# Kernel tuning notes

Hardware: AMD Instinct MI355X
Metric: run time of the kernel (lower is better)

Reference implementation:

```python
import jax, jax.numpy as jnp
import numpy as np
from jax import lax

# ---- module config (init_kwargs) ----
B, CIN, COUT, H, W, K = 16, 32, 32, 256, 256, 3
FEATURE_BITS = 8
INPUT_ZP = 3
OUTPUT_ZP = -5
INPUT_SCALE = 0.02
OUTPUT_SCALE = 0.05
STRIDE = (1, 1)
PAD_H, PAD_W = 1, 1
DILATION = (1, 1)
GROUPS = 1
QMIN, QMAX = -(2 ** (FEATURE_BITS - 1)), 2 ** (FEATURE_BITS - 1) - 1  # -128, 127


def float_to_fixed_point(scale, bitwidth):
    # Represent scale (in (0,1)) as int_scale * 2^-frac_bits with int_scale <= 2^(b-1)-1.
    # Pick the largest frac_bits s.t. round(scale * 2^frac_bits) fits -> max precision.
    qmax = jnp.float32(2 ** (bitwidth - 1) - 1)
    frac_bits = jnp.floor(jnp.log2(qmax / scale)).astype(jnp.int32)
    int_scale = jnp.round(scale * jnp.exp2(frac_bits.astype(jnp.float32))).astype(jnp.int32)
    return int_scale, frac_bits


def setup_inputs() -> dict:
    key = jax.random.key(0)
    k0, k1, k2, k3 = jax.random.split(key, 4)
    x = jax.random.randint(k0, (B, CIN, H, W), -128, 128, dtype=jnp.int32).astype(jnp.int8)
    qweight = jax.random.randint(k1, (COUT, CIN, K, K), -128, 128, dtype=jnp.int32).astype(jnp.int8)
    qbias = jax.random.randint(k2, (COUT,), -1000, 1000, dtype=jnp.int32)
    weight_scale = jax.random.uniform(k3, (COUT,), jnp.float32, 1e-3, 1e-2)
    return {"x": x, "qweight": qweight, "qbias": qbias, "weight_scale": weight_scale}


def reference(x, qweight, qbias, weight_scale):
    # F.pad(qinput, (pw,pw,ph,ph), 'constant', input_zero_point) -> pad W and H dims
    xp = jnp.pad(x, ((0, 0), (0, 0), (PAD_H, PAD_H), (PAD_W, PAD_W)),
                 mode="constant", constant_values=INPUT_ZP)
    # int32 conv (no bias), VALID since input was pre-padded
    out = lax.conv_general_dilated(
        xp.astype(jnp.int32), qweight.astype(jnp.int32),
        window_strides=STRIDE, padding="VALID", rhs_dilation=DILATION,
        dimension_numbers=("NCHW", "OIHW", "NCHW"), feature_group_count=GROUPS)
    # shifted bias: qbias - sum(qweight) * input_zero_point  (per out channel)
    shifted_qbias = qbias - qweight.astype(jnp.int32).sum((1, 2, 3)) * INPUT_ZP
    out = out + shifted_qbias[None, :, None, None]
    # fixed-point requant: (out * int_scale) >> frac_bits, per channel
    folded_scale = (INPUT_SCALE * weight_scale / OUTPUT_SCALE).astype(jnp.float32)
    int_scale, frac_bits = float_to_fixed_point(folded_scale, FEATURE_BITS)
    out = jnp.right_shift(out * int_scale[None, :, None, None],
                          frac_bits[None, :, None, None])  # arithmetic shift on int32
    out = out + OUTPUT_ZP
    out = jnp.clip(out, QMIN, QMAX).astype(jnp.int8)
    return out
```

## Files before the change

kernel.cpp:

```cpp
#include <hip/hip_runtime.h>

#define B_   16
#define CIN  32
#define COUT 32
#define H_   256
#define W_   256
#define IN_ZP  3
#define OUT_ZP (-5)
#define HW (H_ * W_)
#define TH 8
#define TW 64
#define SW 72
#define SH 10

#define XPH 258
#define XPW 264
#define XPQ 66
#define PLANE_W (XPH * XPW)
#define XP_WORDS (B_ * 8 * PLANE_W)
#define WS_TAB 2400
#define WS_NEED ((size_t)(WS_TAB + XP_WORDS) * 4)
#define NQ (B_ * 8 * XPH * XPQ)
#define PACK_BLOCKS 2176


using i32x4  = __attribute__((ext_vector_type(4))) int;
using i32x16 = __attribute__((ext_vector_type(16))) int;


__global__ __launch_bounds__(256) void qconv_pack(const int* __restrict__ x,
                                                  const int* __restrict__ qw,
                                                  const int* __restrict__ qb,
                                                  const float* __restrict__ wscale,
                                                  int* __restrict__ ws) {
    const int bid = blockIdx.x;
    const int tid = threadIdx.x;
    if (bid < 32) {
        __shared__ int red[4];
        const int co = bid;
        const int* wco = qw + co * (CIN * 9);
        int s = 0;
        for (int i = tid; i < CIN * 9; i += 256) s += wco[i];
        for (int off = 32; off; off >>= 1) s += __shfl_down(s, off, 64);
        if ((tid & 63) == 0) red[tid >> 6] = s;

        if (tid < 72) {
            int gidx = co * 72 + tid;
            int g    = gidx & 3;
            int lane = (gidx >> 2) & 63;
            int t    = gidx >> 8;
            int wco2 = lane & 31;
            int ci0  = 16 * (lane >> 5) + 4 * g;
            const int* base = qw + wco2 * (CIN * 9);
            int b0 = base[(ci0 + 0) * 9 + t] & 0xff;
            int b1 = base[(ci0 + 1) * 9 + t] & 0xff;
            int b2 = base[(ci0 + 2) * 9 + t] & 0xff;
            int b3 = base[(ci0 + 3) * 9 + t] & 0xff;
            ws[gidx] = b0 | (b1 << 8) | (b2 << 16) | (b3 << 24);
        }
        __syncthreads();
        if (tid == 0) {
            int wsum = red[0] + red[1] + red[2] + red[3];
            int sb   = qb[co] - wsum * IN_ZP;
            float fs = (0.02f * wscale[co]) / 0.05f;
            float fb = floorf(log2f(127.0f / fs));
            int isc  = (int)rintf(fs * exp2f(fb));
            int ifb  = (int)fb;
            ws[2304 + co] = sb * isc + OUT_ZP * (1 << ifb);
            ws[2336 + co] = isc;
            ws[2368 + co] = ifb;
        }
        return;
    }
    int* __restrict__ xp = ws + WS_TAB;
    const int T = (PACK_BLOCKS) * 256;
    for (int q = (bid - 32) * 256 + tid; q < NQ; q += T) {
        int b   = q / (8 * XPH * XPQ);
        int r1  = q - b * (8 * XPH * XPQ);
        int cig = r1 / (XPH * XPQ);
        int r2  = r1 - cig * (XPH * XPQ);
        int ph  = r2 / XPQ;
        int cq  = r2 - ph * XPQ;
        int gh  = ph - 1;
        int gw0 = cq * 4 - 4;
        int ghc = min(H_ - 1, max(0, gh));
        int gwc = min(W_ - 4, max(0, gw0));
        const int* p = x + (b * CIN + cig * 4) * HW + ghc * W_ + gwc;
        i32x4 v0 = *(const i32x4*)(p);
        i32x4 v1 = *(const i32x4*)(p + HW);
        i32x4 v2 = *(const i32x4*)(p + 2 * HW);
        i32x4 v3 = *(const i32x4*)(p + 3 * HW);
        bool vh = (unsigned)gh < (unsigned)H_;
        i32x4 pk;
#pragma unroll
        for (int j = 0; j < 4; ++j) {
            int t = (v0[j] & 0xff) | ((v1[j] & 0xff) << 8) |
                    ((v2[j] & 0xff) << 16) | (v3[j] << 24);
            bool ok = vh && ((unsigned)(gw0 + j) < (unsigned)W_);
            pk[j] = ok ? t : 0x03030303;
        }
        *(i32x4*)(xp + 4 * q) = pk;
    }
}

__global__ __launch_bounds__(256) void qconv_fused(const int* __restrict__ ws,
                                                   int* __restrict__ out) {
    __shared__ __align__(16) int cons[96];

    const int d  = blockIdx.x + 4 * blockIdx.y + 128 * blockIdx.z;
    const int w  = ((d & 7) << 8) | (d >> 3);
    const int tx = w & 3;
    const int ty = (w >> 2) & 31;
    const int tb = w >> 7;

    const int wt = tx * TW;
    const int ht = ty * TH;
    const int tid = threadIdx.x;
    const int lane = tid & 63, wv = tid >> 6;
    const int hh  = lane >> 5;
    const int pix = lane & 31;
    const int* __restrict__ xp = ws + WS_TAB;

    if (tid < 96) cons[tid] = ws[2304 + tid];

    i32x4 wfrag[9];
    const i32x4* wsv = (const i32x4*)ws;
#pragma unroll
    for (int t = 0; t < 9; ++t) wfrag[t] = wsv[t * 64 + lane];

    __syncthreads();

    const int rowbase = (tb * 8) * XPH + ht;
    const int* xbase = xp + rowbase * XPW + wt + pix + 3;

#pragma unroll 1
    for (int i = 0; i < 4; ++i) {
        const int mt = wv * 4 + i;
        const int r0 = mt >> 1, chunk = mt & 1;
        const int* xt = xbase + (hh * 4) * PLANE_W + r0 * XPW + chunk * 32;
        i32x16 acc;
#pragma unroll
        for (int r = 0; r < 16; ++r) acc[r] = 0;
#pragma unroll
        for (int dh = 0; dh < 3; ++dh) {
#pragma unroll
            for (int dw = 0; dw < 3; ++dw) {
                i32x4 a;
#pragma unroll
                for (int g = 0; g < 4; ++g)
                    a[g] = xt[g * PLANE_W + dh * XPW + dw];
                acc = __builtin_amdgcn_mfma_i32_32x32x32_i8(
                          wfrag[dh * 3 + dw], a, acc, 0, 0, 0);
            }
        }
        int* op = out + (tb * COUT) * HW + (ht + r0) * W_ + wt + chunk * 32 + pix;
#pragma unroll
        for (int rg = 0; rg < 4; ++rg) {
            const int cb = 4 * hh + 8 * rg;
            i32x4 sbi4 = *(const i32x4*)&cons[cb];
            i32x4 isc4 = *(const i32x4*)&cons[32 + cb];
            i32x4 fb4  = *(const i32x4*)&cons[64 + cb];
#pragma unroll
            for (int j = 0; j < 4; ++j) {
                int v = (__mul24(acc[rg * 4 + j], isc4[j]) + sbi4[j]) >> fb4[j];
                v = min(127, max(-128, v));
                __builtin_nontemporal_store(v, op + (cb + j) * HW);
            }
        }
    }
}

__global__ void qconv_prep_fb(const int* __restrict__ qw, const int* __restrict__ qb,
                              const float* __restrict__ wscale, int* __restrict__ ws) {
    const int co  = blockIdx.x;
    const int tid = threadIdx.x;
    __shared__ int red[4];
    const int* wco = qw + co * (CIN * 9);
    int s = 0;
    for (int i = tid; i < CIN * 9; i += 256) s += wco[i];
    for (int off = 32; off; off >>= 1) s += __shfl_down(s, off, 64);
    if ((tid & 63) == 0) red[tid >> 6] = s;
    if (tid < 72) {
        int gidx = blockIdx.x * 72 + tid;
        int g    = gidx & 3;
        int lane = (gidx >> 2) & 63;
        int t    = gidx >> 8;
        int wco2 = lane & 31;
        int ci0  = 16 * (lane >> 5) + 4 * g;
        const int* base = qw + wco2 * (CIN * 9);
        int b0 = base[(ci0 + 0) * 9 + t] & 0xff;
        int b1 = base[(ci0 + 1) * 9 + t] & 0xff;
        int b2 = base[(ci0 + 2) * 9 + t] & 0xff;
        int b3 = base[(ci0 + 3) * 9 + t] & 0xff;
        ws[gidx] = b0 | (b1 << 8) | (b2 << 16) | (b3 << 24);
    }
    __syncthreads();
    if (tid == 0) {
        int wsum = red[0] + red[1] + red[2] + red[3];
        ws[2304 + co] = qb[co] - wsum * IN_ZP;
        float fs = (0.02f * wscale[co]) / 0.05f;
        float fb = floorf(log2f(127.0f / fs));
        int isc = (int)rintf(fs * exp2f(fb));
        ws[2336 + co] = isc | (((int)fb) << 16);
    }
}

__device__ __forceinline__ void stage_item(int idx, int ht, int wt,
                                           const int* __restrict__ xb,
                                           int (*smem)[SH][SW]) {
    int cig = idx / 180;
    int rem = idx - cig * 180;
    int r   = rem / 18;
    int c4  = rem - r * 18;
    int gh  = ht - 1 + r;
    int gw0 = wt - 4 + c4 * 4;
    int ghc = min(H_ - 1, max(0, gh));
    int gwc = min(W_ - 4, max(0, gw0));
    const int* p = xb + (cig * 4) * HW + ghc * W_ + gwc;
    i32x4 v0 = *(const i32x4*)(p);
    i32x4 v1 = *(const i32x4*)(p + HW);
    i32x4 v2 = *(const i32x4*)(p + 2 * HW);
    i32x4 v3 = *(const i32x4*)(p + 3 * HW);
    bool vh = (unsigned)gh < (unsigned)H_;
    i32x4 pk;
#pragma unroll
    for (int j = 0; j < 4; ++j) {
        int t = (v0[j] & 0xff) | ((v1[j] & 0xff) << 8) |
                ((v2[j] & 0xff) << 16) | (v3[j] << 24);
        bool ok = vh && ((unsigned)(gw0 + j) < (unsigned)W_);
        pk[j] = ok ? t : 0x03030303;
    }
    *(i32x4*)&smem[cig][r][c4 * 4] = pk;
}

__global__ __launch_bounds__(256) void qconv_fused_fb(const int* __restrict__ x,
                                                      const int* __restrict__ ws,
                                                      int* __restrict__ out) {
    __shared__ int smem[8][SH][SW];
    __shared__ __align__(16) int cons[64];
    const int d  = blockIdx.x + 4 * blockIdx.y + 128 * blockIdx.z;
    const int w  = ((d & 7) << 8) | (d >> 3);
    const int tx = w & 3;
    const int ty = (w >> 2) & 31;
    const int tb = w >> 7;
    const int wt = tx * TW;
    const int ht = ty * TH;
    const int tid = threadIdx.x;
    const int* xb = x + tb * (CIN * HW);
    if (tid < 64) cons[tid] = ws[2304 + tid];
    stage_item(tid,        ht, wt, xb, smem);
    stage_item(tid + 256,  ht, wt, xb, smem);
    stage_item(tid + 512,  ht, wt, xb, smem);
    stage_item(tid + 768,  ht, wt, xb, smem);
    stage_item(tid + 1024, ht, wt, xb, smem);
    if (tid < 160) stage_item(tid + 1280, ht, wt, xb, smem);
    __syncthreads();
    const int lane = tid & 63, wv = tid >> 6;
    const int hh  = lane >> 5;
    const int pix = lane & 31;
    i32x4 wfrag[9];
    const i32x4* wsv = (const i32x4*)ws;
#pragma unroll
    for (int t = 0; t < 9; ++t) wfrag[t] = wsv[t * 64 + lane];
#pragma unroll
    for (int i = 0; i < 4; ++i) {
        const int mt = wv * 4 + i;
        const int r0 = mt >> 1, chunk = mt & 1;
        i32x16 acc;
#pragma unroll
        for (int r = 0; r < 16; ++r) acc[r] = 0;
#pragma unroll
        for (int t = 0; t < 9; ++t) {
            const int dh = t / 3, dw = t % 3;
            const int rr = r0 + dh;
            const int c  = chunk * 32 + pix + dw + 3;
            i32x4 a;
#pragma unroll
            for (int g = 0; g < 4; ++g) a[g] = smem[4 * hh + g][rr][c];
            acc = __builtin_amdgcn_mfma_i32_32x32x32_i8(wfrag[t], a, acc, 0, 0, 0);
        }
        int* op = out + (tb * COUT) * HW + (ht + r0) * W_ + wt + chunk * 32 + pix;
#pragma unroll
        for (int rg = 0; rg < 4; ++rg) {
            const int cb = 4 * hh + 8 * rg;
            i32x4 sb4 = *(const i32x4*)&cons[cb];
            i32x4 qf4 = *(const i32x4*)&cons[32 + cb];
#pragma unroll
            for (int j = 0; j < 4; ++j) {
                int q = qf4[j];
                int v = acc[rg * 4 + j] + sb4[j];
                v = (int)((unsigned)v * (unsigned)(q & 0xffff)) >> (q >> 16);
                v += OUT_ZP;
                v = min(127, max(-128, v));
                op[(cb + j) * HW] = v;
            }
        }
    }
}

extern "C" void kernel_launch(void* const* d_in, const int* in_sizes, int n_in,
                              void* d_out, int out_size, void* d_ws, size_t ws_size,
                              hipStream_t stream) {
    const int*   x   = (const int*)d_in[0];
    const int*   qw  = (const int*)d_in[1];
    const int*   qb  = (const int*)d_in[2];
    const float* wsc = (const float*)d_in[3];
    int* ws  = (int*)d_ws;
    int* out = (int*)d_out;
    dim3 grid(W_ / TW, H_ / TH, B_);

    if (ws_size >= WS_NEED) {
        qconv_pack<<<32 + PACK_BLOCKS, 256, 0, stream>>>(x, qw, qb, wsc, ws);
        qconv_fused<<<grid, 256, 0, stream>>>(ws, out);
    } else {
        qconv_prep_fb<<<32, 256, 0, stream>>>(qw, qb, wsc, ws);
        qconv_fused_fb<<<grid, 256, 0, stream>>>(x, ws, out);
    }
}
```

Before: 247.6 us.

## Repack padded input to channel-interleaved layout for vector MFMA loads

Measured after the change: 248.9 us. No clear change (+0.5%).

```diff
diff --git a/kernel.cpp b/kernel.cpp
--- a/kernel.cpp
+++ b/kernel.cpp
@@ -15,13 +15,11 @@
 
 #define XPH 258
 #define XPW 264
-#define XPQ 66
-#define PLANE_W (XPH * XPW)
-#define XP_WORDS (B_ * 8 * PLANE_W)
+#define SPATIALS (B_ * XPH * XPW)
+#define XP_WORDS (SPATIALS * 8)
 #define WS_TAB 2400
 #define WS_NEED ((size_t)(WS_TAB + XP_WORDS) * 4)
-#define NQ (B_ * 8 * XPH * XPQ)
-#define PACK_BLOCKS 2176
+#define PACK_BLOCKS (SPATIALS / 256)
 
 
 using i32x4  = __attribute__((ext_vector_type(4))) int;
@@ -73,34 +71,29 @@
         return;
     }
     int* __restrict__ xp = ws + WS_TAB;
-    const int T = (PACK_BLOCKS) * 256;
-    for (int q = (bid - 32) * 256 + tid; q < NQ; q += T) {
-        int b   = q / (8 * XPH * XPQ);
-        int r1  = q - b * (8 * XPH * XPQ);
-        int cig = r1 / (XPH * XPQ);
-        int r2  = r1 - cig * (XPH * XPQ);
-        int ph  = r2 / XPQ;
-        int cq  = r2 - ph * XPQ;
-        int gh  = ph - 1;
-        int gw0 = cq * 4 - 4;
-        int ghc = min(H_ - 1, max(0, gh));
-        int gwc = min(W_ - 4, max(0, gw0));
-        const int* p = x + (b * CIN + cig * 4) * HW + ghc * W_ + gwc;
-        i32x4 v0 = *(const i32x4*)(p);
-        i32x4 v1 = *(const i32x4*)(p + HW);
-        i32x4 v2 = *(const i32x4*)(p + 2 * HW);
-        i32x4 v3 = *(const i32x4*)(p + 3 * HW);
-        bool vh = (unsigned)gh < (unsigned)H_;
-        i32x4 pk;
-#pragma unroll
-        for (int j = 0; j < 4; ++j) {
-            int t = (v0[j] & 0xff) | ((v1[j] & 0xff) << 8) |
-                    ((v2[j] & 0xff) << 16) | (v3[j] << 24);
-            bool ok = vh && ((unsigned)(gw0 + j) < (unsigned)W_);
-            pk[j] = ok ? t : 0x03030303;
-        }
-        *(i32x4*)(xp + 4 * q) = pk;
-    }
+    const int q  = (bid - 32) * 256 + tid;
+    const int b  = q / (XPH * XPW);
+    const int r  = q - b * (XPH * XPW);
+    const int ph = r / XPW;
+    const int pw = r - ph * XPW;
+    const int gh = ph - 1, gw = pw - 4;
+    const int ghc = min(H_ - 1, max(0, gh));
+    const int gwc = min(W_ - 1, max(0, gw));
+    const bool ok = ((unsigned)gh < (unsigned)H_) && ((unsigned)gw < (unsigned)W_);
+    const int* xb = x + b * (CIN * HW) + ghc * W_ + gwc;
+    i32x4 lo, hi;
+#pragma unroll
+    for (int cg = 0; cg < 8; ++cg) {
+        int v0 = xb[(4 * cg + 0) * HW];
+        int v1 = xb[(4 * cg + 1) * HW];
+        int v2 = xb[(4 * cg + 2) * HW];
+        int v3 = xb[(4 * cg + 3) * HW];
+        int pk = (v0 & 0xff) | ((v1 & 0xff) << 8) | ((v2 & 0xff) << 16) | (v3 << 24);
+        pk = ok ? pk : 0x03030303;
+        if (cg < 4) lo[cg] = pk; else hi[cg - 4] = pk;
+    }
+    *(i32x4*)(xp + q * 8)     = lo;
+    *(i32x4*)(xp + q * 8 + 4) = hi;
 }
 
 __global__ __launch_bounds__(256) void qconv_fused(const int* __restrict__ ws,
@@ -130,14 +123,13 @@
 
     __syncthreads();
 
-    const int rowbase = (tb * 8) * XPH + ht;
-    const int* xbase = xp + rowbase * XPW + wt + pix + 3;
+    const int* xbase = xp + ((tb * XPH + ht) * XPW + wt + pix + 3) * 8 + hh * 4;
 
 #pragma unroll 1
     for (int i = 0; i < 4; ++i) {
         const int mt = wv * 4 + i;
         const int r0 = mt >> 1, chunk = mt & 1;
-        const int* xt = xbase + (hh * 4) * PLANE_W + r0 * XPW + chunk * 32;
+        const int* xt = xbase + (r0 * XPW + chunk * 32) * 8;
         i32x16 acc;
 #pragma unroll
         for (int r = 0; r < 16; ++r) acc[r] = 0;
@@ -145,10 +137,7 @@
         for (int dh = 0; dh < 3; ++dh) {
 #pragma unroll
             for (int dw = 0; dw < 3; ++dw) {
-                i32x4 a;
-#pragma unroll
-                for (int g = 0; g < 4; ++g)
-                    a[g] = xt[g * PLANE_W + dh * XPW + dw];
+                i32x4 a = *(const i32x4*)(xt + (dh * XPW + dw) * 8);
                 acc = __builtin_amdgcn_mfma_i32_32x32x32_i8(
                           wfrag[dh * 3 + dw], a, acc, 0, 0, 0);
             }
@@ -244,7 +233,7 @@
     const int ty = (w >> 2) & 31;
     const int tb = w >> 7;
     const int wt = tx * TW;
-    const int ht = ty * TH;
+    const int ht = ty * 8;
     const int tid = threadIdx.x;
     const int* xb = x + tb * (CIN * HW);
     if (tid < 64) cons[tid] = ws[2304 + tid];
@@ -307,13 +296,14 @@
     const float* wsc = (const float*)d_in[3];
     int* ws  = (int*)d_ws;
     int* out = (int*)d_out;
-    dim3 grid(W_ / TW, H_ / TH, B_);
 
     if (ws_size >= WS_NEED) {
         qconv_pack<<<32 + PACK_BLOCKS, 256, 0, stream>>>(x, qw, qb, wsc, ws);
+        dim3 grid(W_ / TW, H_ / TH, B_);
         qconv_fused<<<grid, 256, 0, stream>>>(ws, out);
     } else {
         qconv_prep_fb<<<32, 256, 0, stream>>>(qw, qb, wsc, ws);
-        qconv_fused_fb<<<grid, 256, 0, stream>>>(x, ws, out);
-    }
-}
+        dim3 grid_fb(W_ / TW, H_ / 8, B_);
+        qconv_fused_fb<<<grid_fb, 256, 0, stream>>>(x, ws, out);
+    }
+}
```
